# Optimization experiments

Hardware: AMD Instinct MI355X
Metric: run time of the kernel (lower is better)

Reference implementation:

```python
import jax, jax.numpy as jnp
import numpy as np

EPS = 1e-12  # matches torch F.normalize default eps

def _l2_normalize(v, axis):
    n = jnp.sqrt(jnp.sum(v * v, axis=axis, keepdims=True))
    return v / jnp.maximum(n, EPS)

def setup_inputs() -> dict:
    key = jax.random.key(0)
    k1, k2, k3 = jax.random.split(key, 3)
    N, C, H, W = 16, 128, 64, 64
    D, K = 512, 64
    x = jax.random.normal(k1, (N, C, H, W), dtype=jnp.float32)
    conv_w = jax.random.normal(k2, (D, C), dtype=jnp.float32) * (1.0 / np.sqrt(C))
    conv_b = jnp.zeros((D,), dtype=jnp.float32)
    centroids = jax.random.uniform(k3, (K, D), dtype=jnp.float32)
    return {"x": x, "conv_w": conv_w, "conv_b": conv_b, "centroids": centroids}

def reference(x, conv_w, conv_b, centroids):
    N, C, H, W = x.shape
    D = conv_w.shape[0]
    # descriptor-wise L2 normalization over channels
    x = _l2_normalize(x, axis=1)
    # 1x1 conv == per-pixel linear projection; flatten spatial -> L = H*W
    f = jnp.einsum('nchw,dc->ndhw', x, conv_w) + conv_b[None, :, None, None]
    f = f.reshape(N, D, H * W)                      # (N, D, L)
    c = _l2_normalize(centroids, axis=1)            # (K, D)
    # soft assignment: dot of normalized centroid with each projected descriptor
    logits = jnp.einsum('kd,ndl->nkl', c, f)        # (N, K, L)
    s = jax.nn.softmax(logits, axis=-1)             # softmax over spatial positions
    # weighted sum of descriptors per cluster (no (N,K,D,L) materialization)
    vlad = jnp.einsum('nkl,ndl->nkd', s, f)         # (N, K, D)
    return vlad
```

## Files before the change

kernel.cpp:

```cpp
#include <hip/hip_runtime.h>

#define NB 16
#define CD 128
#define HW 4096
#define DD 512
#define KC 64

typedef __attribute__((ext_vector_type(8))) short bfrag;
typedef __attribute__((ext_vector_type(4))) float facc;

__device__ __forceinline__ unsigned short f2bf(float f) {
  union { float f; unsigned u; } v; v.f = f;
  unsigned r = v.u + 0x7fffu + ((v.u >> 16) & 1u);
  return (unsigned short)(r >> 16);
}
__device__ __forceinline__ float bf2f(unsigned short h) {
  union { unsigned u; float f; } v; v.u = ((unsigned)h) << 16; return v.f;
}
__device__ __forceinline__ unsigned f2bf2(float lo, float hi) {
  unsigned r;
  asm("v_cvt_pk_bf16_f32 %0, %1, %2" : "=v"(r) : "v"(lo), "v"(hi));
  return r;
}
__device__ __forceinline__ void gll16(const void* g, void* l) {
  __builtin_amdgcn_global_load_lds(
      (__attribute__((address_space(1))) void*)(uintptr_t)g,
      (__attribute__((address_space(3))) void*)(uintptr_t)l, 16, 0, 0);
}
__device__ __forceinline__ int swzr(int r) { return ((r & 7) ^ ((r >> 3) & 7)) << 4; }

__global__ __launch_bounds__(256) void k_prep(const float* __restrict__ conv_w,
                                              const float* __restrict__ centroids,
                                              unsigned short* __restrict__ Wsw,
                                              unsigned short* __restrict__ Cbsw) {
  int b = blockIdx.x, t = threadIdx.x;
  if (b < KC) {
    const float* row = centroids + (size_t)b * DD;
    float v0 = row[t], v1 = row[t + 256];
    float ss = v0 * v0 + v1 * v1;
    #pragma unroll
    for (int off = 32; off; off >>= 1) ss += __shfl_xor(ss, off);
    __shared__ float red[4];
    if ((t & 63) == 0) red[t >> 6] = ss;
    __syncthreads();
    float tot = red[0] + red[1] + red[2] + red[3];
    float inv = 1.0f / fmaxf(sqrtf(tot), 1e-12f);
    int d0 = t, d1 = t + 256;
    *(unsigned short*)((char*)Cbsw + (d0 >> 6) * 8192 + b * 128 +
                       (((d0 & 63) * 2) ^ swzr(b))) = f2bf(v0 * inv);
    *(unsigned short*)((char*)Cbsw + (d1 >> 6) * 8192 + b * 128 +
                       (((d1 & 63) * 2) ^ swzr(b))) = f2bf(v1 * inv);
  } else {
    int i = (b - KC) * 2048 + t * 8;
    const float4* src = (const float4*)(conv_w + i);
    float4 a = src[0], c4 = src[1];
    int d = i >> 7, c0 = i & 127;
    int dch = d >> 6, dl = d & 63;
    uint4 w;
    w.x = f2bf2(a.x, a.y);   w.y = f2bf2(a.z, a.w);
    w.z = f2bf2(c4.x, c4.y); w.w = f2bf2(c4.z, c4.w);
    *(uint4*)((char*)Wsw + dch * 16384 + dl * 256 + ((c0 * 2) ^ swzr(dl))) = w;
  }
}

__global__ __launch_bounds__(512, 2) void k_xproj(const float* __restrict__ x,
                                                  const unsigned short* __restrict__ Wsw,
                                                  const unsigned short* __restrict__ Cbsw,
                                                  const float* __restrict__ conv_b,
                                                  unsigned short* __restrict__ fT,
                                                  unsigned short* __restrict__ eg,
                                                  float* __restrict__ psums) {
  __shared__ __align__(16) char smem[67072];
  char* Xraw  = smem;
  char* fbuf  = smem;
  char* etile = smem + 16384;
  char* Ws    = smem + 32768;
  char* Cb2   = smem + 49152;
  float* invb = (float*)(smem + 65536);
  float* ps   = (float*)(smem + 66048);
  int n = blockIdx.y, lblk = blockIdx.x, l0 = lblk * 128;
  int t = threadIdx.x, lane = t & 63, wid = t >> 6;

  #pragma unroll
  for (int q = 0; q < 2; q++)
    gll16((const char*)Wsw + (q * 8 + wid) * 1024 + lane * 16, Ws + (q * 8 + wid) * 1024);
  gll16((const char*)Cbsw + wid * 1024 + lane * 16, Cb2 + wid * 1024);

  #pragma unroll
  for (int j = 0; j < 2; j++) {
    int c0 = ((t >> 4) + 32 * j) * 2;
    const float4* r0p = (const float4*)(x + ((size_t)n * CD + c0) * HW + l0);
    const float4* r1p = (const float4*)(x + ((size_t)n * CD + c0 + 1) * HW + l0);
    #pragma unroll
    for (int jj = 0; jj < 2; jj++) {
      int f4 = (t & 15) + 16 * jj;
      float4 a = r0p[f4], b = r1p[f4];
      int lb = f4 * 4;
      *(unsigned*)(Xraw + (lb + 0) * 256 + ((c0 * 2) ^ swzr(lb + 0))) = f2bf2(a.x, b.x);
      *(unsigned*)(Xraw + (lb + 1) * 256 + ((c0 * 2) ^ swzr(lb + 1))) = f2bf2(a.y, b.y);
      *(unsigned*)(Xraw + (lb + 2) * 256 + ((c0 * 2) ^ swzr(lb + 2))) = f2bf2(a.z, b.z);
      *(unsigned*)(Xraw + (lb + 3) * 256 + ((c0 * 2) ^ swzr(lb + 3))) = f2bf2(a.w, b.w);
    }
  }
  __syncthreads();

  {
    int l = t >> 2;
    float ss = 0.f;
    #pragma unroll
    for (int p = 0; p < 4; p++) {
      int s16 = (t & 3) + 4 * p;
      bfrag v = *(const bfrag*)(Xraw + l * 256 + ((s16 * 16) ^ swzr(l)));
      #pragma unroll
      for (int i = 0; i < 8; i++) { float f = bf2f((unsigned short)v[i]); ss += f * f; }
    }
    ss += __shfl_xor(ss, 1); ss += __shfl_xor(ss, 2);
    if ((t & 3) == 0) invb[l] = 1.0f / fmaxf(sqrtf(ss), 1e-12f);
  }
  __syncthreads();

  int wd = wid & 1, wl = wid >> 1;
  int er = wid >> 2, ec = wid & 3;
  int r0 = (lane >> 4) << 2, cl = lane & 15;
  int hi8 = (lane >> 4) << 3;

  bfrag bfh[4][2];
  #pragma unroll
  for (int kk = 0; kk < 4; kk++)
    #pragma unroll
    for (int j = 0; j < 2; j++) {
      int row = wl * 32 + j * 16 + cl;
      int c0e = kk * 32 + hi8;
      bfh[kk][j] = *(const bfrag*)(Xraw + row * 256 + ((c0e * 2) ^ swzr(row)));
    }
  float hinv[2];
  #pragma unroll
  for (int j = 0; j < 2; j++) hinv[j] = invb[wl * 32 + j * 16 + cl];
  __syncthreads();

  facc zero = {0.f, 0.f, 0.f, 0.f};
  facc e_acc[2][2];
  e_acc[0][0] = zero; e_acc[0][1] = zero; e_acc[1][0] = zero; e_acc[1][1] = zero;

  for (int dch = 0; dch < 8; dch++) {
    const char* Cbs = Cb2 + ((dch & 1) << 13);
    facc acc[2][2];
    acc[0][0] = zero; acc[0][1] = zero; acc[1][0] = zero; acc[1][1] = zero;
    #pragma unroll
    for (int kk = 0; kk < 4; kk++) {
      int c0e = kk * 32 + hi8;
      bfrag am[2];
      #pragma unroll
      for (int m = 0; m < 2; m++) {
        int d = wd * 32 + m * 16 + cl;
        am[m] = *(const bfrag*)(Ws + d * 256 + ((c0e * 2) ^ swzr(d)));
      }
      #pragma unroll
      for (int m = 0; m < 2; m++)
        #pragma unroll
        for (int j = 0; j < 2; j++)
          acc[m][j] = __builtin_amdgcn_mfma_f32_16x16x32_bf16(am[m], bfh[kk][j], acc[m][j], 0, 0, 0);
    }
    #pragma unroll
    for (int m = 0; m < 2; m++) {
      int d0 = wd * 32 + m * 16 + r0;
      float4 bq = *(const float4*)(conv_b + dch * 64 + d0);
      #pragma unroll
      for (int j = 0; j < 2; j++) {
        int l = wl * 32 + j * 16 + cl;
        uint2 w;
        w.x = f2bf2(acc[m][j][0] * hinv[j] + bq.x, acc[m][j][1] * hinv[j] + bq.y);
        w.y = f2bf2(acc[m][j][2] * hinv[j] + bq.z, acc[m][j][3] * hinv[j] + bq.w);
        *(uint2*)(fbuf + l * 128 + ((d0 * 2) ^ swzr(l))) = w;
      }
    }
    asm volatile("s_waitcnt vmcnt(2) lgkmcnt(0)" ::: "memory");
    __builtin_amdgcn_s_barrier();
    __builtin_amdgcn_sched_barrier(0);
    if (dch < 7) {
      #pragma unroll
      for (int q = 0; q < 2; q++)
        gll16((const char*)Wsw + (dch + 1) * 16384 + (q * 8 + wid) * 1024 + lane * 16,
              Ws + (q * 8 + wid) * 1024);
      gll16((const char*)Cbsw + (dch + 1) * 8192 + wid * 1024 + lane * 16,
            Cb2 + (((dch + 1) & 1) << 13) + wid * 1024);
    }
    __builtin_amdgcn_sched_barrier(0);
    {
      #pragma unroll
      for (int p = 0; p < 2; p++) {
        int ch = p * 512 + t;
        int lr = ch >> 3, c16 = ch & 7;
        bfrag v = *(const bfrag*)(fbuf + lr * 128 + ((c16 * 16) ^ swzr(lr)));
        *(bfrag*)(fT + ((size_t)n * HW + l0 + lr) * DD + dch * 64 + c16 * 8) = v;
      }
    }
    #pragma unroll
    for (int kk = 0; kk < 2; kk++) {
      int d0 = kk * 32 + hi8;
      bfrag ca[2], fb[2];
      #pragma unroll
      for (int m2 = 0; m2 < 2; m2++) {
        int k2 = er * 32 + m2 * 16 + cl;
        ca[m2] = *(const bfrag*)(Cbs + k2 * 128 + ((d0 * 2) ^ swzr(k2)));
      }
      #pragma unroll
      for (int j2 = 0; j2 < 2; j2++) {
        int l2 = ec * 32 + j2 * 16 + cl;
        fb[j2] = *(const bfrag*)(fbuf + l2 * 128 + ((d0 * 2) ^ swzr(l2)));
      }
      #pragma unroll
      for (int m2 = 0; m2 < 2; m2++)
        #pragma unroll
        for (int j2 = 0; j2 < 2; j2++)
          e_acc[m2][j2] = __builtin_amdgcn_mfma_f32_16x16x32_bf16(ca[m2], fb[j2], e_acc[m2][j2], 0, 0, 0);
    }
    asm volatile("s_waitcnt vmcnt(3) lgkmcnt(0)" ::: "memory");
    __builtin_amdgcn_s_barrier();
    __builtin_amdgcn_sched_barrier(0);
  }

  {
    int l2base = ec * 32;
    #pragma unroll
    for (int m2 = 0; m2 < 2; m2++) {
      #pragma unroll
      for (int q = 0; q < 4; q++) {
        int k2 = er * 32 + m2 * 16 + r0 + q;
        float vsum = 0.f;
        #pragma unroll
        for (int j2 = 0; j2 < 2; j2++) {
          int l2 = l2base + j2 * 16 + cl;
          float ev = __expf(e_acc[m2][j2][q]);
          *(unsigned short*)(etile + (l2 >> 6) * 8192 + k2 * 128 +
                             (((l2 & 63) * 2) ^ swzr(k2))) = f2bf(ev);
          vsum += ev;
        }
        vsum += __shfl_xor(vsum, 1); vsum += __shfl_xor(vsum, 2);
        vsum += __shfl_xor(vsum, 4); vsum += __shfl_xor(vsum, 8);
        if (cl == 0) ps[k2 * 4 + ec] = vsum;
      }
    }
  }
  __syncthreads();
  {
    size_t base = ((size_t)n * 64 + lblk * 2) * 8192;
    #pragma unroll
    for (int p = 0; p < 2; p++) {
      uint4 v = *(const uint4*)(etile + (t + p * 512) * 16);
      *(uint4*)((char*)eg + base + (t + p * 512) * 16) = v;
    }
  }
  if (t < 64) {
    float4 v = ((const float4*)ps)[t];
    psums[((size_t)n * 32 + lblk) * 64 + t] = v.x + v.y + v.z + v.w;
  }
}

__global__ __launch_bounds__(256) void k_vlad(const unsigned short* __restrict__ eg,
                                              const unsigned short* __restrict__ fT,
                                              float* __restrict__ part) {
  __shared__ __align__(16) char smem[49152];
  char* As = smem;
  char* Bs = smem + 16384;
  int t = threadIdx.x, lane = t & 63, wid = t >> 6;
  int wr = wid >> 1, wc = wid & 1;
  int lin = blockIdx.x;
  int xcd = lin & 7, jj = lin >> 3;
  int grp = xcd * 8 + (jj >> 2);
  int dt = jj & 3, n = grp >> 2, sk = grp & 3;
  int dbase = dt * 128;
  facc acc[2][4];
  facc zero = {0.f, 0.f, 0.f, 0.f};
  #pragma unroll
  for (int m = 0; m < 2; m++)
    #pragma unroll
    for (int j = 0; j < 4; j++) acc[m][j] = zero;

  for (int ks = 0; ks < 8; ks++) {
    int l0 = sk * 1024 + ks * 128;
    {
      const char* easrc = (const char*)eg + ((size_t)n * 64 + (l0 >> 6)) * 8192;
      #pragma unroll
      for (int q = 0; q < 4; q++)
        gll16(easrc + (q * 4 + wid) * 1024 + lane * 16, As + (q * 4 + wid) * 1024);
    }
    #pragma unroll
    for (int q = 0; q < 8; q++) {
      int ch = q * 256 + t;
      int l = ch >> 4, dc = ch & 15;
      bfrag v = *(const bfrag*)(fT + ((size_t)n * HW + l0 + l) * DD + dbase + dc * 8);
      #pragma unroll
      for (int i = 0; i < 8; i++) {
        int d = dc * 8 + i;
        int swz = (((d & 7) ^ ((d >> 3) & 7)) << 4);
        *(unsigned short*)(Bs + d * 256 + ((l * 2) ^ swz)) = (unsigned short)v[i];
      }
    }
    __syncthreads();
    #pragma unroll
    for (int kk = 0; kk < 128; kk += 32) {
      int lk = kk + ((lane >> 4) << 3);
      const char* Ai = As + (kk >> 6) * 8192;
      int ll = lk & 63;
      bfrag af[2], bf[4];
      #pragma unroll
      for (int m = 0; m < 2; m++) {
        int krow = wr * 32 + m * 16 + (lane & 15);
        af[m] = *(const bfrag*)(Ai + krow * 128 + ((ll * 2) ^ swzr(krow)));
      }
      #pragma unroll
      for (int j = 0; j < 4; j++) {
        int d = wc * 64 + j * 16 + (lane & 15);
        int swz = (((d & 7) ^ ((d >> 3) & 7)) << 4);
        bf[j] = *(const bfrag*)(Bs + d * 256 + ((lk * 2) ^ swz));
      }
      #pragma unroll
      for (int m = 0; m < 2; m++)
        #pragma unroll
        for (int j = 0; j < 4; j++)
          acc[m][j] = __builtin_amdgcn_mfma_f32_16x16x32_bf16(af[m], bf[j], acc[m][j], 0, 0, 0);
    }
    __syncthreads();
  }
  int r0 = (lane >> 4) << 2, cl = lane & 15;
  size_t base = ((size_t)(sk * NB + n)) * (KC * DD);
  #pragma unroll
  for (int m = 0; m < 2; m++) {
    int krow = wr * 32 + m * 16 + r0;
    #pragma unroll
    for (int j = 0; j < 4; j++) {
      int d = dbase + wc * 64 + j * 16 + cl;
      #pragma unroll
      for (int q = 0; q < 4; q++)
        part[base + (size_t)(krow + q) * DD + d] = acc[m][j][q];
    }
  }
}

__global__ __launch_bounds__(256) void k_reduce(const float* __restrict__ part,
                                                const float* __restrict__ psums,
                                                float* __restrict__ out) {
  int b = blockIdx.x, t = threadIdx.x;
  int nk = b >> 1;
  int n = nk >> 6, k = nk & 63;
  __shared__ float rsh;
  if (t < 32) {
    float s = psums[((size_t)n * 32 + t) * 64 + k];
    #pragma unroll
    for (int off = 16; off; off >>= 1) s += __shfl_xor(s, off, 32);
    if (t == 0) rsh = 1.0f / s;
  }
  __syncthreads();
  float rinv = rsh;
  int i = b * 256 + t;
  float s = 0.f;
  #pragma unroll
  for (int skk = 0; skk < 4; skk++) s += part[(size_t)skk * (NB * KC * DD) + i];
  out[i] = s * rinv;
}

extern "C" void kernel_launch(void* const* d_in, const int* in_sizes, int n_in,
                              void* d_out, int out_size, void* d_ws, size_t ws_size,
                              hipStream_t stream) {
  const float* x         = (const float*)d_in[0];
  const float* conv_w    = (const float*)d_in[1];
  const float* conv_b    = (const float*)d_in[2];
  const float* centroids = (const float*)d_in[3];
  float* out = (float*)d_out;
  char* ws = (char*)d_ws;

  unsigned short* Wsw  = (unsigned short*)(ws);
  unsigned short* Cbsw = (unsigned short*)(ws + 131072);
  unsigned short* fT   = (unsigned short*)(ws + 196608);
  unsigned short* eg   = (unsigned short*)(ws + 67305472ull);
  float*          psums= (float*)(ws + 75694080ull);
  float*          part = (float*)(ws + 75960320ull);

  k_prep<<<dim3(96), dim3(256), 0, stream>>>(conv_w, centroids, Wsw, Cbsw);

  k_xproj<<<dim3(32, NB), dim3(512), 0, stream>>>(x, Wsw, Cbsw, conv_b, fT, eg, psums);

  k_vlad<<<dim3(256), dim3(256), 0, stream>>>(eg, fT, part);

  k_reduce<<<dim3(NB * KC * DD / 256), dim3(256), 0, stream>>>(part, psums, out);

  (void)in_sizes; (void)n_in; (void)out_size; (void)ws_size;
}
```

Baseline: 58.40 us.

## Double the split-K in VLAD GEMM and prefetch next fT tile in registers

```diff
diff --git a/kernel.cpp b/kernel.cpp
--- a/kernel.cpp
+++ b/kernel.cpp
@@ -257,9 +257,9 @@
   }
 }
 
-__global__ __launch_bounds__(256) void k_vlad(const unsigned short* __restrict__ eg,
-                                              const unsigned short* __restrict__ fT,
-                                              float* __restrict__ part) {
+__global__ __launch_bounds__(256, 2) void k_vlad(const unsigned short* __restrict__ eg,
+                                                 const unsigned short* __restrict__ fT,
+                                                 float* __restrict__ part) {
   __shared__ __align__(16) char smem[49152];
   char* As = smem;
   char* Bs = smem + 16384;
@@ -267,9 +267,10 @@
   int wr = wid >> 1, wc = wid & 1;
   int lin = blockIdx.x;
   int xcd = lin & 7, jj = lin >> 3;
-  int grp = xcd * 8 + (jj >> 2);
-  int dt = jj & 3, n = grp >> 2, sk = grp & 3;
+  int grp = xcd * 16 + (jj >> 2);
+  int dt = jj & 3, n = grp >> 3, sk = grp & 7;
   int dbase = dt * 128;
+  const unsigned short* fTb = fT + (size_t)n * HW * DD + dbase;
   facc acc[2][4];
   facc zero = {0.f, 0.f, 0.f, 0.f};
   #pragma unroll
@@ -277,27 +278,49 @@
     #pragma unroll
     for (int j = 0; j < 4; j++) acc[m][j] = zero;
 
-  for (int ks = 0; ks < 8; ks++) {
-    int l0 = sk * 1024 + ks * 128;
-    {
-      const char* easrc = (const char*)eg + ((size_t)n * 64 + (l0 >> 6)) * 8192;
-      #pragma unroll
-      for (int q = 0; q < 4; q++)
-        gll16(easrc + (q * 4 + wid) * 1024 + lane * 16, As + (q * 4 + wid) * 1024);
-    }
+  bfrag br[8];
+  #pragma unroll
+  for (int q = 0; q < 8; q++) {
+    int ch = q * 256 + t;
+    int l = ch >> 4, dc = ch & 15;
+    br[q] = *(const bfrag*)(fTb + (size_t)(sk * 512 + l) * DD + dc * 8);
+  }
+
+  #pragma unroll
+  for (int ks = 0; ks < 4; ks++) {
+    int l0 = sk * 512 + ks * 128;
     #pragma unroll
     for (int q = 0; q < 8; q++) {
       int ch = q * 256 + t;
       int l = ch >> 4, dc = ch & 15;
-      bfrag v = *(const bfrag*)(fT + ((size_t)n * HW + l0 + l) * DD + dbase + dc * 8);
       #pragma unroll
       for (int i = 0; i < 8; i++) {
         int d = dc * 8 + i;
         int swz = (((d & 7) ^ ((d >> 3) & 7)) << 4);
-        *(unsigned short*)(Bs + d * 256 + ((l * 2) ^ swz)) = (unsigned short)v[i];
-      }
-    }
-    __syncthreads();
+        *(unsigned short*)(Bs + d * 256 + ((l * 2) ^ swz)) = (unsigned short)br[q][i];
+      }
+    }
+    __builtin_amdgcn_sched_barrier(0);
+    {
+      const char* easrc = (const char*)eg + ((size_t)n * 64 + (l0 >> 6)) * 8192;
+      #pragma unroll
+      for (int q = 0; q < 4; q++)
+        gll16(easrc + (q * 4 + wid) * 1024 + lane * 16, As + (q * 4 + wid) * 1024);
+    }
+    __builtin_amdgcn_sched_barrier(0);
+    if (ks < 3) {
+      #pragma unroll
+      for (int q = 0; q < 8; q++) {
+        int ch = q * 256 + t;
+        int l = ch >> 4, dc = ch & 15;
+        br[q] = *(const bfrag*)(fTb + (size_t)(l0 + 128 + l) * DD + dc * 8);
+      }
+      asm volatile("s_waitcnt vmcnt(8) lgkmcnt(0)" ::: "memory");
+    } else {
+      asm volatile("s_waitcnt vmcnt(0) lgkmcnt(0)" ::: "memory");
+    }
+    __builtin_amdgcn_s_barrier();
+    __builtin_amdgcn_sched_barrier(0);
     #pragma unroll
     for (int kk = 0; kk < 128; kk += 32) {
       int lk = kk + ((lane >> 4) << 3);
@@ -321,7 +344,9 @@
         for (int j = 0; j < 4; j++)
           acc[m][j] = __builtin_amdgcn_mfma_f32_16x16x32_bf16(af[m], bf[j], acc[m][j], 0, 0, 0);
     }
-    __syncthreads();
+    asm volatile("s_waitcnt lgkmcnt(0)" ::: "memory");
+    __builtin_amdgcn_s_barrier();
+    __builtin_amdgcn_sched_barrier(0);
   }
   int r0 = (lane >> 4) << 2, cl = lane & 15;
   size_t base = ((size_t)(sk * NB + n)) * (KC * DD);
@@ -356,7 +381,7 @@
   int i = b * 256 + t;
   float s = 0.f;
   #pragma unroll
-  for (int skk = 0; skk < 4; skk++) s += part[(size_t)skk * (NB * KC * DD) + i];
+  for (int skk = 0; skk < 8; skk++) s += part[(size_t)skk * (NB * KC * DD) + i];
   out[i] = s * rinv;
 }
 
@@ -381,7 +406,7 @@
 
   k_xproj<<<dim3(32, NB), dim3(512), 0, stream>>>(x, Wsw, Cbsw, conv_b, fT, eg, psums);
 
-  k_vlad<<<dim3(256), dim3(256), 0, stream>>>(eg, fT, part);
+  k_vlad<<<dim3(512), dim3(256), 0, stream>>>(eg, fT, part);
 
   k_reduce<<<dim3(NB * KC * DD / 256), dim3(256), 0, stream>>>(part, psums, out);
 
```

Result: faster. 54.78 us (median of 2 runs) (-6.2%).
